# Kernel tuning notes

Hardware: AMD Instinct MI355X
Metric: run time of the kernel (lower is better)

## Reference

```python
import jax, jax.numpy as jnp
import numpy as np

BATCH, H, W = 1024, 32, 32
NUM_PIXELS = H * W                 # 1024
NUM_WIRES = 11                     # ceil(log2(1024)) + 1
NUM_LAYERS = 8

_CNOT = jnp.array([[1, 0, 0, 0],
                   [0, 1, 0, 0],
                   [0, 0, 0, 1],
                   [0, 0, 1, 0]], dtype=jnp.complex64)


def setup_inputs() -> dict:
    key = jax.random.key(0)
    k1, k2, k3 = jax.random.split(key, 3)
    image = jax.random.uniform(k1, (BATCH, 1, H, W), dtype=jnp.float32)
    label = jax.random.normal(k2, (BATCH,), dtype=jnp.float32)
    weights = jax.random.normal(k3, (NUM_LAYERS, NUM_WIRES, 3), dtype=jnp.float32) * 0.4
    return {"image": image, "label": label, "weights": weights}


def _apply_1q(state, U, w):
    # state: (B,) + (2,)*n ; U: (2,2) shared or (B,2,2) per-batch
    st = jnp.moveaxis(state, w + 1, -1)
    if U.ndim == 3:
        out = jnp.einsum('bij,b...j->b...i', U, st)
    else:
        out = jnp.einsum('ij,...j->...i', U, st)
    return jnp.moveaxis(out, -1, w + 1)


def _apply_cnot(state, c, t):
    last = state.ndim - 1
    st = jnp.moveaxis(state, (c + 1, t + 1), (last - 1, last))
    sh = st.shape
    st = st.reshape(sh[:-2] + (4,)) @ _CNOT.T
    st = st.reshape(sh)
    return jnp.moveaxis(st, (last - 1, last), (c + 1, t + 1))


def _rot(phi, theta, omega):
    # PennyLane Rot = RZ(omega) RY(theta) RZ(phi)
    c = jnp.cos(theta / 2).astype(jnp.complex64)
    s = jnp.sin(theta / 2).astype(jnp.complex64)
    ep = jnp.exp(-0.5j * (phi + omega))
    em = jnp.exp(0.5j * (phi - omega))
    return jnp.array([[ep * c, -em * s],
                      [jnp.conj(em) * s, jnp.conj(ep) * c]])


def _circuit(image, label, weights):
    B = image.shape[0]
    x = image.reshape(B, NUM_PIXELS)
    # AmplitudeEmbedding(normalize=True) on wires 0..NUM_WIRES-2; ancilla wire in |0>
    psi = x / jnp.linalg.norm(x, axis=1, keepdims=True)
    state = jnp.zeros((B, 2 ** NUM_WIRES), jnp.complex64)
    state = state.at[:, ::2].set(psi.astype(jnp.complex64))  # ancilla = least-significant wire
    state = state.reshape((B,) + (2,) * NUM_WIRES)

    # RX(label) on the last wire (per-batch angle)
    c = jnp.cos(label / 2).astype(jnp.complex64)
    s = (-1j * jnp.sin(label / 2)).astype(jnp.complex64)
    rx = jnp.stack([jnp.stack([c, s], -1), jnp.stack([s, c], -1)], -2)  # (B,2,2)
    state = _apply_1q(state, rx, NUM_WIRES - 1)

    # weights remapped as in the module
    wr = jnp.pi * jnp.tanh(weights)

    # StronglyEntanglingLayers: per layer, Rot on every wire then ring of CNOTs with range r
    for l in range(NUM_LAYERS):
        for q in range(NUM_WIRES):
            state = _apply_1q(state, _rot(wr[l, q, 0], wr[l, q, 1], wr[l, q, 2]), q)
        r = (l % (NUM_WIRES - 1)) + 1
        for q in range(NUM_WIRES):
            state = _apply_cnot(state, q, (q + r) % NUM_WIRES)

    probs = jnp.abs(state.reshape(B, -1)) ** 2          # (B, 2048)
    probs = probs[:, ::2]                               # ancilla == 0 outcomes, (B, 1024)
    out = probs * NUM_PIXELS                            # decode: undo 1/num_pixels scale
    return out.reshape(B, 1, H, W)


def reference(image, label, weights):
    return _circuit(image, label, weights)
```

## Files before the change

kernel.cpp:

```cpp
#include <hip/hip_runtime.h>
#include <math.h>

#define NW 11
#define NL 8
#define NPIX 1024
#define TPB 128

typedef float f2 __attribute__((ext_vector_type(2)));
typedef float f4 __attribute__((ext_vector_type(4)));

__device__ __forceinline__ int SW(int i) { return i ^ (((i >> 4) & 7) << 1); }

__device__ __forceinline__ int Fmap(int m, int r) {
    #pragma unroll
    for (int q = 0; q < NW; ++q) {
        int pc = 10 - q;
        int qq = q + r; if (qq >= NW) qq -= NW;
        int pt = 10 - qq;
        m ^= ((m >> pc) & 1) << pt;
    }
    return m;
}

template<int B>
__device__ __forceinline__ void gate16(f2 (&v)[16], const f2* __restrict__ g) {
    f2 c0 = g[0], c1 = g[1], c2 = g[2], c3 = g[3];
    f2 c4 = g[4], c5 = g[5], c6 = g[6], c7 = g[7];
    #pragma unroll
    for (int s = 0; s < 16; ++s) {
        if (s & B) continue;
        f2 v0 = v[s], v1 = v[s | B];
        f2 w0 = v0.yx, w1 = v1.yx;
        f2 o0 = __builtin_elementwise_fma(c3, w1,
                 __builtin_elementwise_fma(c2, v1,
                  __builtin_elementwise_fma(c1, w0, c0 * v0)));
        f2 o1 = __builtin_elementwise_fma(c7, w1,
                 __builtin_elementwise_fma(c6, v1,
                  __builtin_elementwise_fma(c5, w0, c4 * v0)));
        v[s] = o0; v[s | B] = o1;
    }
}

__global__ void gates_kernel(const float* __restrict__ weights, f2* __restrict__ gw) {
    int t = threadIdx.x;
    if (t < NL * NW) {
        const float* w = weights + t * 3;
        const float PI = 3.14159265358979323846f;
        float phi   = PI * tanhf(w[0]);
        float theta = PI * tanhf(w[1]);
        float omega = PI * tanhf(w[2]);
        float ct = cosf(0.5f * theta), st = sinf(0.5f * theta);
        float a  = 0.5f * (phi + omega), bb = 0.5f * (phi - omega);
        float ca = cosf(a), sa = sinf(a), cb = cosf(bb), sb = sinf(bb);
        float u00r =  ca * ct, u00i = -sa * ct;
        float u01r = -cb * st, u01i = -sb * st;
        float u10r =  cb * st, u10i = -sb * st;
        float u11r =  ca * ct, u11i =  sa * ct;
        f2* g = gw + t * 8;
        g[0] = (f2){u00r, u00r}; g[1] = (f2){-u00i, u00i};
        g[2] = (f2){u01r, u01r}; g[3] = (f2){-u01i, u01i};
        g[4] = (f2){u10r, u10r}; g[5] = (f2){-u10i, u10i};
        g[6] = (f2){u11r, u11r}; g[7] = (f2){-u11i, u11i};
    }
}

__global__ __launch_bounds__(TPB) void pqc_kernel(
    const float* __restrict__ image, const float* __restrict__ label,
    const f2* __restrict__ gw, float* __restrict__ out)
{
    __shared__ __align__(16) f2 sS[2048];
    __shared__ int sColS[NL * NW];
    __shared__ int sD16[NL * 16];
    __shared__ float sRed[2];

    const int b = blockIdx.x, t = threadIdx.x;

    const f4* img4 = (const f4*)(image + (size_t)b * NPIX);
    f4 x0 = img4[2 * t], x1 = img4[2 * t + 1];

    if (t < NL * NW) {
        int l = t / NW, p = t % NW;
        sColS[t] = SW(Fmap(1 << p, l + 1));
    }

    float ss = x0.x*x0.x + x0.y*x0.y + x0.z*x0.z + x0.w*x0.w
             + x1.x*x1.x + x1.y*x1.y + x1.z*x1.z + x1.w*x1.w;
    #pragma unroll
    for (int off = 32; off >= 1; off >>= 1) ss += __shfl_down(ss, off);
    if ((t & 63) == 0) sRed[t >> 6] = ss;
    __syncthreads();

    {
        int l = t >> 4, s = t & 15;
        int d = 0;
        if (s & 1) d ^= sColS[l * NW + 0];
        if (s & 2) d ^= sColS[l * NW + 8];
        if (s & 4) d ^= sColS[l * NW + 9];
        if (s & 8) d ^= sColS[l * NW + 10];
        sD16[t] = d;
    }

    const float inv = 1.0f / sqrtf(sRed[0] + sRed[1]);
    const float lab = label[b];
    const float cl = cosf(0.5f * lab), sl = sinf(0.5f * lab);

    {
        const int base = t << 4, key2 = (t & 7) << 1;
        float ps[8] = {x0.x, x0.y, x0.z, x0.w, x1.x, x1.y, x1.z, x1.w};
        #pragma unroll
        for (int j = 0; j < 8; ++j) {
            float p = ps[j] * inv;
            f4 w; w.x = cl * p; w.y = 0.f; w.z = 0.f; w.w = -sl * p;
            *(f4*)&sS[base + ((2 * j) ^ key2)] = w;
        }
    }
    __syncthreads();

    f2 v[16];
    for (int l = 0; l < NL; ++l) {
        const f2* G = gw + (size_t)l * NW * 8;

        {
            const int base = t << 4, key2 = (t & 7) << 1;
            #pragma unroll
            for (int k = 0; k < 8; ++k) {
                f4 w = *(const f4*)&sS[base + ((2 * k) ^ key2)];
                v[2*k] = w.xy; v[2*k+1] = w.zw;
            }
            gate16<1>(v, G + 10 * 8);
            gate16<2>(v, G +  9 * 8);
            gate16<4>(v, G +  8 * 8);
            gate16<8>(v, G +  7 * 8);
            #pragma unroll
            for (int k = 0; k < 8; ++k) {
                f4 w; w.xy = v[2*k]; w.zw = v[2*k+1];
                *(f4*)&sS[base + ((2 * k) ^ key2)] = w;
            }
        }
        __syncthreads();

        {
            const int base = (t & 15) | ((t >> 4) << 8);
            #pragma unroll
            for (int s = 0; s < 16; ++s)
                v[s] = sS[(base ^ ((s & 7) << 1)) + (s << 4)];
            gate16<1>(v, G + 6 * 8);
            gate16<2>(v, G + 5 * 8);
            gate16<4>(v, G + 4 * 8);
            gate16<8>(v, G + 3 * 8);
            #pragma unroll
            for (int s = 0; s < 16; ++s)
                sS[(base ^ ((s & 7) << 1)) + (s << 4)] = v[s];
        }
        __syncthreads();

        {
            const int base = t << 1;
            const int eb = base ^ (((t >> 3) & 7) << 1);
            #pragma unroll
            for (int k = 0; k < 8; ++k) {
                f4 w = *(const f4*)&sS[eb + (k << 8)];
                v[2*k] = w.xy; v[2*k+1] = w.zw;
            }
            gate16<2>(v, G + 2 * 8);
            gate16<4>(v, G + 1 * 8);
            gate16<8>(v, G + 0 * 8);
            int swMB = 0;
            #pragma unroll
            for (int p = 1; p <= 7; ++p)
                if ((base >> p) & 1) swMB ^= sColS[l * NW + p];
            const int* D = &sD16[l * 16];
            #pragma unroll
            for (int s = 0; s < 16; ++s)
                sS[swMB ^ D[s]] = v[s];
        }
        __syncthreads();
    }

    {
        const int eb = (2 * t) ^ (((t >> 3) & 7) << 1);
        #pragma unroll
        for (int k = 0; k < 8; ++k) {
            f2 a = sS[eb + (k << 8)];
            out[(size_t)b * NPIX + (k << 7) + t] = (a.x*a.x + a.y*a.y) * (float)NPIX;
        }
    }
}

extern "C" void kernel_launch(void* const* d_in, const int* in_sizes, int n_in,
                              void* d_out, int out_size, void* d_ws, size_t ws_size,
                              hipStream_t stream) {
    const float* image   = (const float*)d_in[0];
    const float* label   = (const float*)d_in[1];
    const float* weights = (const float*)d_in[2];
    float* out = (float*)d_out;
    f2* gw = (f2*)d_ws;
    int batch = in_sizes[1];
    gates_kernel<<<1, TPB, 0, stream>>>(weights, gw);
    pqc_kernel<<<batch, TPB, 0, stream>>>(image, label, gw, out);
}
```

Baseline: 44.22 us.

## Use 256 threads with 8 amplitudes each and host-precomputed CNOT permutation tables

Doubles threads per block to 256, so each thread holds 8 amplitudes instead of 16. Each layer now runs in four passes of three (or two) wire gates instead of three passes of four. The CNOT-ring permutation tables are computed on the host and passed as a kernel argument, replacing the per-block shared-memory table setup, and a new swizzle avoids bank conflicts. The initial state is kept in registers rather than written to shared memory first. This trades more parallelism and lower register pressure for one extra barrier and shared-memory round trip per layer.

Result: no change. 45.06 us (+1.9%).

```diff
diff --git a/kernel.cpp b/kernel.cpp
--- a/kernel.cpp
+++ b/kernel.cpp
@@ -4,15 +4,14 @@
 #define NW 11
 #define NL 8
 #define NPIX 1024
-#define TPB 128
+#define TPB 256
 
 typedef float f2 __attribute__((ext_vector_type(2)));
 typedef float f4 __attribute__((ext_vector_type(4)));
 
-__device__ __forceinline__ int SW(int i) { return i ^ (((i >> 4) & 7) << 1); }
-
-__device__ __forceinline__ int Fmap(int m, int r) {
-    #pragma unroll
+struct PermTab { int fe[NL][8]; int d[NL][8]; };
+
+__host__ __device__ inline int fmap_h(int m, int r) {
     for (int q = 0; q < NW; ++q) {
         int pc = 10 - q;
         int qq = q + r; if (qq >= NW) qq -= NW;
@@ -22,12 +21,16 @@
     return m;
 }
 
+__host__ __device__ constexpr int SW(int e) {
+    return e ^ (((e >> 3) & 7) << 1) ^ (((e >> 6) & 1) << 3);
+}
+
 template<int B>
-__device__ __forceinline__ void gate16(f2 (&v)[16], const f2* __restrict__ g) {
+__device__ __forceinline__ void gate8(f2 (&v)[8], const f2* __restrict__ g) {
     f2 c0 = g[0], c1 = g[1], c2 = g[2], c3 = g[3];
     f2 c4 = g[4], c5 = g[5], c6 = g[6], c7 = g[7];
     #pragma unroll
-    for (int s = 0; s < 16; ++s) {
+    for (int s = 0; s < 8; ++s) {
         if (s & B) continue;
         f2 v0 = v[s], v1 = v[s | B];
         f2 w0 = v0.yx, w1 = v1.yx;
@@ -66,124 +69,108 @@
 
 __global__ __launch_bounds__(TPB) void pqc_kernel(
     const float* __restrict__ image, const float* __restrict__ label,
-    const f2* __restrict__ gw, float* __restrict__ out)
+    const f2* __restrict__ gw, float* __restrict__ out, PermTab pt)
 {
     __shared__ __align__(16) f2 sS[2048];
-    __shared__ int sColS[NL * NW];
-    __shared__ int sD16[NL * 16];
-    __shared__ float sRed[2];
+    __shared__ float sRed[4];
 
     const int b = blockIdx.x, t = threadIdx.x;
 
-    const f4* img4 = (const f4*)(image + (size_t)b * NPIX);
-    f4 x0 = img4[2 * t], x1 = img4[2 * t + 1];
-
-    if (t < NL * NW) {
-        int l = t / NW, p = t % NW;
-        sColS[t] = SW(Fmap(1 << p, l + 1));
-    }
-
-    float ss = x0.x*x0.x + x0.y*x0.y + x0.z*x0.z + x0.w*x0.w
-             + x1.x*x1.x + x1.y*x1.y + x1.z*x1.z + x1.w*x1.w;
+    const f4 x = ((const f4*)(image + (size_t)b * NPIX))[t];
+    float ss = x.x * x.x + x.y * x.y + x.z * x.z + x.w * x.w;
     #pragma unroll
     for (int off = 32; off >= 1; off >>= 1) ss += __shfl_down(ss, off);
     if ((t & 63) == 0) sRed[t >> 6] = ss;
     __syncthreads();
-
-    {
-        int l = t >> 4, s = t & 15;
-        int d = 0;
-        if (s & 1) d ^= sColS[l * NW + 0];
-        if (s & 2) d ^= sColS[l * NW + 8];
-        if (s & 4) d ^= sColS[l * NW + 9];
-        if (s & 8) d ^= sColS[l * NW + 10];
-        sD16[t] = d;
-    }
-
-    const float inv = 1.0f / sqrtf(sRed[0] + sRed[1]);
+    const float inv = 1.0f / sqrtf(sRed[0] + sRed[1] + sRed[2] + sRed[3]);
+
     const float lab = label[b];
     const float cl = cosf(0.5f * lab), sl = sinf(0.5f * lab);
 
+    f2 v[8];
     {
-        const int base = t << 4, key2 = (t & 7) << 1;
-        float ps[8] = {x0.x, x0.y, x0.z, x0.w, x1.x, x1.y, x1.z, x1.w};
+        float ps[4] = {x.x, x.y, x.z, x.w};
         #pragma unroll
-        for (int j = 0; j < 8; ++j) {
-            float p = ps[j] * inv;
-            f4 w; w.x = cl * p; w.y = 0.f; w.z = 0.f; w.w = -sl * p;
-            *(f4*)&sS[base + ((2 * j) ^ key2)] = w;
-        }
-    }
-    __syncthreads();
-
-    f2 v[16];
+        for (int m = 0; m < 4; ++m) {
+            float p = ps[m] * inv;
+            v[2 * m]     = (f2){cl * p, 0.f};
+            v[2 * m + 1] = (f2){0.f, -sl * p};
+        }
+    }
+
+    const int swb0 = SW(t << 3);
+    const int swb1 = SW((t & 7) | ((t >> 3) << 6));
+    const int swb2 = SW((t & 63) | ((t >> 6) << 9));
+    const int swb3 = SW(t << 1);
+
     for (int l = 0; l < NL; ++l) {
         const f2* G = gw + (size_t)l * NW * 8;
 
+        if (l) {
+            #pragma unroll
+            for (int k = 0; k < 4; ++k) {
+                f4 w = *(const f4*)&sS[swb0 ^ SW(2 * k)];
+                v[2 * k] = w.xy; v[2 * k + 1] = w.zw;
+            }
+        }
+        gate8<1>(v, G + 10 * 8);
+        gate8<2>(v, G +  9 * 8);
+        gate8<4>(v, G +  8 * 8);
+        #pragma unroll
+        for (int k = 0; k < 4; ++k) {
+            f4 w; w.xy = v[2 * k]; w.zw = v[2 * k + 1];
+            *(f4*)&sS[swb0 ^ SW(2 * k)] = w;
+        }
+        __syncthreads();
+
         {
-            const int base = t << 4, key2 = (t & 7) << 1;
-            #pragma unroll
-            for (int k = 0; k < 8; ++k) {
-                f4 w = *(const f4*)&sS[base + ((2 * k) ^ key2)];
-                v[2*k] = w.xy; v[2*k+1] = w.zw;
+            #pragma unroll
+            for (int s = 0; s < 8; ++s) v[s] = sS[swb1 ^ SW(s << 3)];
+            gate8<1>(v, G + 7 * 8);
+            gate8<2>(v, G + 6 * 8);
+            gate8<4>(v, G + 5 * 8);
+            #pragma unroll
+            for (int s = 0; s < 8; ++s) sS[swb1 ^ SW(s << 3)] = v[s];
+        }
+        __syncthreads();
+
+        {
+            #pragma unroll
+            for (int s = 0; s < 8; ++s) v[s] = sS[swb2 ^ SW(s << 6)];
+            gate8<1>(v, G + 4 * 8);
+            gate8<2>(v, G + 3 * 8);
+            gate8<4>(v, G + 2 * 8);
+            #pragma unroll
+            for (int s = 0; s < 8; ++s) sS[swb2 ^ SW(s << 6)] = v[s];
+        }
+        __syncthreads();
+
+        {
+            #pragma unroll
+            for (int k = 0; k < 4; ++k) {
+                f4 w = *(const f4*)&sS[swb3 ^ ((k & 1) << 9) ^ ((k >> 1) << 10)];
+                v[2 * k] = w.xy; v[2 * k + 1] = w.zw;
             }
-            gate16<1>(v, G + 10 * 8);
-            gate16<2>(v, G +  9 * 8);
-            gate16<4>(v, G +  8 * 8);
-            gate16<8>(v, G +  7 * 8);
-            #pragma unroll
-            for (int k = 0; k < 8; ++k) {
-                f4 w; w.xy = v[2*k]; w.zw = v[2*k+1];
-                *(f4*)&sS[base + ((2 * k) ^ key2)] = w;
-            }
-        }
-        __syncthreads();
-
-        {
-            const int base = (t & 15) | ((t >> 4) << 8);
-            #pragma unroll
-            for (int s = 0; s < 16; ++s)
-                v[s] = sS[(base ^ ((s & 7) << 1)) + (s << 4)];
-            gate16<1>(v, G + 6 * 8);
-            gate16<2>(v, G + 5 * 8);
-            gate16<4>(v, G + 4 * 8);
-            gate16<8>(v, G + 3 * 8);
-            #pragma unroll
-            for (int s = 0; s < 16; ++s)
-                sS[(base ^ ((s & 7) << 1)) + (s << 4)] = v[s];
-        }
-        __syncthreads();
-
-        {
-            const int base = t << 1;
-            const int eb = base ^ (((t >> 3) & 7) << 1);
-            #pragma unroll
-            for (int k = 0; k < 8; ++k) {
-                f4 w = *(const f4*)&sS[eb + (k << 8)];
-                v[2*k] = w.xy; v[2*k+1] = w.zw;
-            }
-            gate16<2>(v, G + 2 * 8);
-            gate16<4>(v, G + 1 * 8);
-            gate16<8>(v, G + 0 * 8);
-            int swMB = 0;
-            #pragma unroll
-            for (int p = 1; p <= 7; ++p)
-                if ((base >> p) & 1) swMB ^= sColS[l * NW + p];
-            const int* D = &sD16[l * 16];
-            #pragma unroll
-            for (int s = 0; s < 16; ++s)
-                sS[swMB ^ D[s]] = v[s];
+            gate8<2>(v, G + 1 * 8);
+            gate8<4>(v, G + 0 * 8);
+            int msw = 0;
+            #pragma unroll
+            for (int k2 = 0; k2 < 8; ++k2)
+                msw ^= ((t >> k2) & 1) ? pt.fe[l][k2] : 0;
+            #pragma unroll
+            for (int s = 0; s < 8; ++s) sS[msw ^ pt.d[l][s]] = v[s];
         }
         __syncthreads();
     }
 
     {
-        const int eb = (2 * t) ^ (((t >> 3) & 7) << 1);
+        f4 o;
         #pragma unroll
-        for (int k = 0; k < 8; ++k) {
-            f2 a = sS[eb + (k << 8)];
-            out[(size_t)b * NPIX + (k << 7) + t] = (a.x*a.x + a.y*a.y) * (float)NPIX;
-        }
+        for (int k = 0; k < 4; ++k) {
+            f2 a = sS[swb0 ^ SW(2 * k)];
+            ((float*)&o)[k] = (a.x * a.x + a.y * a.y) * (float)NPIX;
+        }
+        ((f4*)(out + (size_t)b * NPIX))[t] = o;
     }
 }
 
@@ -195,7 +182,22 @@
     const float* weights = (const float*)d_in[2];
     float* out = (float*)d_out;
     f2* gw = (f2*)d_ws;
+
+    PermTab pt;
+    for (int l = 0; l < NL; ++l) {
+        int r = l + 1;
+        for (int k = 0; k < 8; ++k)
+            pt.fe[l][k] = SW(fmap_h(1 << (k + 1), r));
+        for (int s = 0; s < 8; ++s) {
+            int m = 0;
+            if (s & 1) m ^= fmap_h(1,       r);
+            if (s & 2) m ^= fmap_h(1 << 9,  r);
+            if (s & 4) m ^= fmap_h(1 << 10, r);
+            pt.d[l][s] = SW(m);
+        }
+    }
+
     int batch = in_sizes[1];
-    gates_kernel<<<1, TPB, 0, stream>>>(weights, gw);
-    pqc_kernel<<<batch, TPB, 0, stream>>>(image, label, gw, out);
-}
+    gates_kernel<<<1, 128, 0, stream>>>(weights, gw);
+    pqc_kernel<<<batch, TPB, 0, stream>>>(image, label, gw, out, pt);
+}
```
